# Performance work log

Measured on AMD Instinct MI355X. Metric: run time of the kernel, lower is better.

## Reference

```python
import jax, jax.numpy as jnp
import numpy as np

D = 16  # attention temperature
COEF = 1.0 / float(np.sqrt(D))


def squash2(x, axis=-1):
    sq = jnp.sum(x * x, axis=axis, keepdims=True)
    norm = jnp.sqrt(sq)
    # (1 - 1/exp(||x||)) * x / sqrt(||x||^2 + 1e-8)
    return (1.0 - jnp.exp(-norm)) * x / jnp.sqrt(sq + 1e-8)


def setup_inputs() -> dict:
    key = jax.random.key(0)
    k1, k2, k3 = jax.random.split(key, 3)
    batch, in_caps, in_dim, num_caps, dim_caps = 128, 1024, 16, 16, 16
    x = jax.random.normal(k1, (batch, in_caps, in_dim), dtype=jnp.float32)
    W = 0.01 * jax.random.normal(k2, (1, num_caps, in_caps, dim_caps, in_dim), dtype=jnp.float32)
    B = 0.01 * jax.random.normal(k3, (num_caps, 1, in_caps), dtype=jnp.float32)
    return {"x": x, "W": W, "B": B}


def reference(x, W, B):
    # u_hat[b,n,c,d] = W[n,c,d,:] . x[b,c,:]
    u_hat = jnp.einsum('ncdi,bci->bncd', W[0], x)
    # a = coef * u_hat @ u_hat^T is only consumed via a.sum(dim=-2);
    # sum_r <u_hat[r], u_hat[k]> == <sum_r u_hat[r], u_hat[k]> (same math, no [c,c] matrix)
    scores = COEF * jnp.einsum('bnd,bnkd->bnk', u_hat.sum(axis=2), u_hat)  # [b,n,c]
    c = jax.nn.softmax(scores[:, :, None, :], axis=1)  # softmax over num_caps, [b,n,1,c]
    # s = (c + B) @ u_hat, squeeze row dim
    s = jnp.einsum('bnrc,bncd->bnrd', c + B[None], u_hat)[:, :, 0, :]  # [b,n,d]
    return squash2(s)
```

## Files before the change

kernel.cpp:

```cpp
#include <hip/hip_runtime.h>
#include <math.h>

#define NB 128
#define NC 1024
#define NN 16
#define ND 16
#define NI 16
#define COEF 0.25f

typedef __attribute__((ext_vector_type(8))) short short8;
typedef __attribute__((ext_vector_type(4))) float f32x4;
typedef unsigned short ushort_t;

__device__ __forceinline__ unsigned short f2bf(float f) {
  unsigned int u = __builtin_bit_cast(unsigned int, f);
  u += 0x7fffu + ((u >> 16) & 1u);
  return (unsigned short)(u >> 16);
}

__global__ __launch_bounds__(256) void k_prep(const float4* __restrict__ x,
                                              const float4* __restrict__ W,
                                              ushort_t* __restrict__ xb,
                                              ushort_t* __restrict__ Wb) {
  int id = blockIdx.x * 256 + threadIdx.x;
  const float4* src;
  ushort_t* dst;
  int k;
  if (id < 262144) { src = x; dst = xb; k = id; }
  else { src = W; dst = Wb; k = id - 262144; }
  float4 a = src[2 * k], b = src[2 * k + 1];
  short8 o;
  o[0] = (short)f2bf(a.x); o[1] = (short)f2bf(a.y);
  o[2] = (short)f2bf(a.z); o[3] = (short)f2bf(a.w);
  o[4] = (short)f2bf(b.x); o[5] = (short)f2bf(b.y);
  o[6] = (short)f2bf(b.z); o[7] = (short)f2bf(b.w);
  *(short8*)(dst + (size_t)k * 8) = o;
}

__global__ __launch_bounds__(1024) void k_usum(const ushort_t* __restrict__ xb,
                                               const ushort_t* __restrict__ Wb,
                                               float* __restrict__ usum2) {
  __shared__ f32x4 red[16][64];
  int bx = blockIdx.x;
  int bt = bx >> 5, g = bx & 31;
  int n = g >> 1, h = g & 1;
  int w = threadIdx.x >> 6, l = threadIdx.x & 63;
  int q = l >> 4, b16 = l & 15;
  int c0 = h * 512 + w * 32;
  f32x4 acc[4];
#pragma unroll
  for (int kk = 0; kk < 4; ++kk) acc[kk] = (f32x4){0.f, 0.f, 0.f, 0.f};
#pragma unroll
  for (int kk = 0; kk < 4; ++kk) {
    const ushort_t* ap =
        Wb + (((size_t)(n * NC + c0 + kk * 8 + (q >> 1)) * ND + b16) * NI) + (q & 1) * 8;
    const ushort_t* bp =
        xb + (size_t)(bt * 16 + b16) * (NC * NI) + (c0 + kk * 8 + (q >> 1)) * NI + (q & 1) * 8;
#pragma unroll
    for (int s = 0; s < 4; ++s) {
      short8 av = *(const short8*)ap;
      short8 bv = *(const short8*)bp;
      acc[kk] = __builtin_amdgcn_mfma_f32_16x16x32_bf16(av, bv, acc[kk], 0, 0, 0);
      ap += 2 * ND * NI;
      bp += 2 * NI;
    }
  }
  red[w][l] = (acc[0] + acc[1]) + (acc[2] + acc[3]);
  __syncthreads();
  if (threadIdx.x < 64) {
    f32x4 t = red[0][l];
#pragma unroll
    for (int k = 1; k < 16; ++k) t += red[k][l];
    *(f32x4*)(usum2 + (((size_t)h * NN + n) * NB + bt * 16 + b16) * ND + q * 4) = t;
  }
}

__global__ __launch_bounds__(512, 4) void k_bc(const ushort_t* __restrict__ xb,
                                               const ushort_t* __restrict__ Wb,
                                               const float* __restrict__ usum2,
                                               const float* __restrict__ Bbias,
                                               float* __restrict__ part) {
  __shared__ ushort_t Wl[NN][8][ND][NI];
  __shared__ ushort_t xl[16][136];
  __shared__ float scl[NN][8][16];
  int bx = blockIdx.x;
  int bt = bx >> 7, cc = bx & 127;
  int t = threadIdx.x;
  int w = t >> 6, l = t & 63;
  int q = l >> 4, b16 = l & 15;
  int c0 = cc * 8;
  int n0 = w, n1 = w + 8;

  const float* u0p = usum2 + ((size_t)n0 * NB + bt * 16 + b16) * ND + q * 4;
  f32x4 us0 = *(const f32x4*)u0p + *(const f32x4*)(u0p + (size_t)NN * NB * ND);
  const float* u1p = usum2 + ((size_t)n1 * NB + bt * 16 + b16) * ND + q * 4;
  f32x4 us1 = *(const f32x4*)u1p + *(const f32x4*)(u1p + (size_t)NN * NB * ND);

  {
    ushort_t* Wflat = &Wl[0][0][0][0];
    const ushort_t* Wsrc = Wb + (size_t)c0 * (ND * NI);
#pragma unroll
    for (int r = 0; r < 8; ++r) {
      int g = r * 512 + t;
      int n = g >> 8, rem = g & 255;
      *(short8*)(Wflat + n * 2048 + rem * 8) =
          *(const short8*)(Wsrc + (size_t)n * (NC * ND * NI) + rem * 8);
    }
    if (t < 256) {
      int b = t >> 4, j = t & 15;
      int c = j >> 1, i8 = j & 1;
      *(short8*)(&xl[b][c * 16 + i8 * 8]) =
          *(const short8*)(xb + ((size_t)(bt * 16 + b) * NC + c0 + c) * NI + i8 * 8);
    }
  }
  __syncthreads();

  f32x4 t0[8], t1[8];

#pragma unroll
  for (int c = 0; c < 8; ++c) {
    short8 av = {0, 0, 0, 0, 0, 0, 0, 0};
    short8 bv = {0, 0, 0, 0, 0, 0, 0, 0};
    if (q < 2) {
      av = *(const short8*)(&Wl[n0][c][b16][q * 8]);
      bv = *(const short8*)(&xl[b16][c * 16 + q * 8]);
    }
    f32x4 z = {0.f, 0.f, 0.f, 0.f};
    f32x4 d = __builtin_amdgcn_mfma_f32_16x16x32_bf16(av, bv, z, 0, 0, 0);
    t0[c] = d;
    float v = us0[0] * d[0] + us0[1] * d[1] + us0[2] * d[2] + us0[3] * d[3];
    v += __shfl_xor(v, 16);
    v += __shfl_xor(v, 32);
    if (l < 16) scl[n0][c][l] = COEF * v;
  }
#pragma unroll
  for (int c = 0; c < 8; ++c) {
    short8 av = {0, 0, 0, 0, 0, 0, 0, 0};
    short8 bv = {0, 0, 0, 0, 0, 0, 0, 0};
    if (q < 2) {
      av = *(const short8*)(&Wl[n1][c][b16][q * 8]);
      bv = *(const short8*)(&xl[b16][c * 16 + q * 8]);
    }
    f32x4 z = {0.f, 0.f, 0.f, 0.f};
    f32x4 d = __builtin_amdgcn_mfma_f32_16x16x32_bf16(av, bv, z, 0, 0, 0);
    t1[c] = d;
    float v = us1[0] * d[0] + us1[1] * d[1] + us1[2] * d[2] + us1[3] * d[3];
    v += __shfl_xor(v, 16);
    v += __shfl_xor(v, 32);
    if (l < 16) scl[n1][c][l] = COEF * v;
  }
  __syncthreads();

  if (t < 128) {
    int c = t >> 4, b = t & 15;
    float v[NN];
    float m = -1e30f;
#pragma unroll
    for (int k = 0; k < NN; ++k) {
      v[k] = scl[k][c][b];
      m = fmaxf(m, v[k]);
    }
    float sum = 0.f;
#pragma unroll
    for (int k = 0; k < NN; ++k) {
      v[k] = expf(v[k] - m);
      sum += v[k];
    }
    float inv = 1.0f / sum;
#pragma unroll
    for (int k = 0; k < NN; ++k) {
      scl[k][c][b] = v[k] * inv + Bbias[k * NC + c0 + c];
    }
  }
  __syncthreads();

  f32x4 acc0 = {0.f, 0.f, 0.f, 0.f};
  f32x4 acc1 = {0.f, 0.f, 0.f, 0.f};
#pragma unroll
  for (int c = 0; c < 8; ++c) {
    float cf0 = scl[n0][c][b16];
    float cf1 = scl[n1][c][b16];
    acc0[0] = fmaf(cf0, t0[c][0], acc0[0]);
    acc0[1] = fmaf(cf0, t0[c][1], acc0[1]);
    acc0[2] = fmaf(cf0, t0[c][2], acc0[2]);
    acc0[3] = fmaf(cf0, t0[c][3], acc0[3]);
    acc1[0] = fmaf(cf1, t1[c][0], acc1[0]);
    acc1[1] = fmaf(cf1, t1[c][1], acc1[1]);
    acc1[2] = fmaf(cf1, t1[c][2], acc1[2]);
    acc1[3] = fmaf(cf1, t1[c][3], acc1[3]);
  }
  *(f32x4*)(part + ((size_t)((n0 * 8 + bt) * 128 + cc)) * 256 + b16 * 16 + q * 4) = acc0;
  *(f32x4*)(part + ((size_t)((n1 * 8 + bt) * 128 + cc)) * 256 + b16 * 16 + q * 4) = acc1;
}

__global__ __launch_bounds__(256) void k_fin(const float* __restrict__ part,
                                             float* __restrict__ out) {
  int id2 = blockIdx.x * 256 + threadIdx.x;
  int h = id2 & 1;
  int id = id2 >> 1;
  int dq = id & 3, n = (id >> 2) & 15, b = id >> 6;
  int bt = b >> 4, b16 = b & 15;
  f32x4 sv = {0.f, 0.f, 0.f, 0.f};
  const float* pp = part + ((size_t)((n * 8 + bt) * 128 + h * 64)) * 256 + b16 * 16 + dq * 4;
  for (int k = 0; k < 64; ++k) {
    sv += *(const f32x4*)pp;
    pp += 256;
  }
  sv[0] += __shfl_xor(sv[0], 1);
  sv[1] += __shfl_xor(sv[1], 1);
  sv[2] += __shfl_xor(sv[2], 1);
  sv[3] += __shfl_xor(sv[3], 1);
  float sq = sv[0] * sv[0] + sv[1] * sv[1] + sv[2] * sv[2] + sv[3] * sv[3];
  sq += __shfl_xor(sq, 2);
  sq += __shfl_xor(sq, 4);
  float norm = sqrtf(sq);
  float scale = (1.0f - expf(-norm)) / sqrtf(sq + 1e-8f);
  if (h == 0) {
    f32x4 o = {sv[0] * scale, sv[1] * scale, sv[2] * scale, sv[3] * scale};
    *(f32x4*)(out + (size_t)id * 4) = o;
  }
}

extern "C" void kernel_launch(void* const* d_in, const int* in_sizes, int n_in,
                              void* d_out, int out_size, void* d_ws, size_t ws_size,
                              hipStream_t stream) {
  const float* x = (const float*)d_in[0];
  const float* W = (const float*)d_in[1];
  const float* Bb = (const float*)d_in[2];
  float* out = (float*)d_out;
  float* ws = (float*)d_ws;

  ushort_t* xb = (ushort_t*)ws;
  ushort_t* Wb = (ushort_t*)(ws + 1048576);
  float* part = ws + 1048576 + 2097152;
  float* usum2 = part + 4194304;

  hipLaunchKernelGGL(k_prep, dim3(3072), dim3(256), 0, stream,
                     (const float4*)x, (const float4*)W, xb, Wb);
  hipLaunchKernelGGL(k_usum, dim3(256), dim3(1024), 0, stream, xb, Wb, usum2);
  hipLaunchKernelGGL(k_bc, dim3(1024), dim3(512), 0, stream, xb, Wb, usum2, Bb, part);
  hipLaunchKernelGGL(k_fin, dim3(64), dim3(256), 0, stream, part, out);
}
```

Baseline: 48.42 us.

## Fuse bf16 conversion into usum kernel and restructure final reduction

Drops the separate fp32-to-bf16 prep kernel. The usum kernel now reads fp32 x and W directly, converts them in registers, and writes the bf16 copies for the next stage: W only from the bt==0 blocks and x only from the n==0 blocks. This removes one launch and one full pass over the inputs, but the usum kernel now reads fp32 data redundantly across blocks. The final kernel is also rebuilt to use 128 blocks of 512 threads, with coalesced scalar reads of the partials and a shared-memory combine of the two halves.

```diff
diff --git a/kernel.cpp b/kernel.cpp
--- a/kernel.cpp
+++ b/kernel.cpp
@@ -18,27 +18,19 @@
   return (unsigned short)(u >> 16);
 }
 
-__global__ __launch_bounds__(256) void k_prep(const float4* __restrict__ x,
-                                              const float4* __restrict__ W,
-                                              ushort_t* __restrict__ xb,
-                                              ushort_t* __restrict__ Wb) {
-  int id = blockIdx.x * 256 + threadIdx.x;
-  const float4* src;
-  ushort_t* dst;
-  int k;
-  if (id < 262144) { src = x; dst = xb; k = id; }
-  else { src = W; dst = Wb; k = id - 262144; }
-  float4 a = src[2 * k], b = src[2 * k + 1];
+__device__ __forceinline__ short8 cvt8(float4 a, float4 b) {
   short8 o;
   o[0] = (short)f2bf(a.x); o[1] = (short)f2bf(a.y);
   o[2] = (short)f2bf(a.z); o[3] = (short)f2bf(a.w);
   o[4] = (short)f2bf(b.x); o[5] = (short)f2bf(b.y);
   o[6] = (short)f2bf(b.z); o[7] = (short)f2bf(b.w);
-  *(short8*)(dst + (size_t)k * 8) = o;
-}
-
-__global__ __launch_bounds__(1024) void k_usum(const ushort_t* __restrict__ xb,
-                                               const ushort_t* __restrict__ Wb,
+  return o;
+}
+
+__global__ __launch_bounds__(1024) void k_usum(const float* __restrict__ xf,
+                                               const float* __restrict__ Wf,
+                                               ushort_t* __restrict__ xb,
+                                               ushort_t* __restrict__ Wb,
                                                float* __restrict__ usum2) {
   __shared__ f32x4 red[16][64];
   int bx = blockIdx.x;
@@ -47,22 +39,28 @@
   int w = threadIdx.x >> 6, l = threadIdx.x & 63;
   int q = l >> 4, b16 = l & 15;
   int c0 = h * 512 + w * 32;
+  const bool writeW = (bt == 0);
+  const bool writeX = (n == 0);
   f32x4 acc[4];
 #pragma unroll
   for (int kk = 0; kk < 4; ++kk) acc[kk] = (f32x4){0.f, 0.f, 0.f, 0.f};
 #pragma unroll
   for (int kk = 0; kk < 4; ++kk) {
-    const ushort_t* ap =
-        Wb + (((size_t)(n * NC + c0 + kk * 8 + (q >> 1)) * ND + b16) * NI) + (q & 1) * 8;
-    const ushort_t* bp =
-        xb + (size_t)(bt * 16 + b16) * (NC * NI) + (c0 + kk * 8 + (q >> 1)) * NI + (q & 1) * 8;
+    size_t wo = (((size_t)(n * NC + c0 + kk * 8 + (q >> 1)) * ND + b16) * NI) + (q & 1) * 8;
+    size_t xo = ((size_t)(bt * 16 + b16) * NC + (c0 + kk * 8 + (q >> 1))) * NI + (q & 1) * 8;
 #pragma unroll
     for (int s = 0; s < 4; ++s) {
-      short8 av = *(const short8*)ap;
-      short8 bv = *(const short8*)bp;
+      float4 w0 = *(const float4*)(Wf + wo);
+      float4 w1 = *(const float4*)(Wf + wo + 4);
+      float4 x0 = *(const float4*)(xf + xo);
+      float4 x1 = *(const float4*)(xf + xo + 4);
+      short8 av = cvt8(w0, w1);
+      short8 bv = cvt8(x0, x1);
+      if (writeW) *(short8*)(Wb + wo) = av;
+      if (writeX) *(short8*)(xb + xo) = bv;
       acc[kk] = __builtin_amdgcn_mfma_f32_16x16x32_bf16(av, bv, acc[kk], 0, 0, 0);
-      ap += 2 * ND * NI;
-      bp += 2 * NI;
+      wo += 2 * ND * NI;
+      xo += 2 * NI;
     }
   }
   red[w][l] = (acc[0] + acc[1]) + (acc[2] + acc[3]);
@@ -193,31 +191,33 @@
   *(f32x4*)(part + ((size_t)((n1 * 8 + bt) * 128 + cc)) * 256 + b16 * 16 + q * 4) = acc1;
 }
 
-__global__ __launch_bounds__(256) void k_fin(const float* __restrict__ part,
+__global__ __launch_bounds__(512) void k_fin(const float* __restrict__ part,
                                              float* __restrict__ out) {
-  int id2 = blockIdx.x * 256 + threadIdx.x;
-  int h = id2 & 1;
-  int id = id2 >> 1;
-  int dq = id & 3, n = (id >> 2) & 15, b = id >> 6;
-  int bt = b >> 4, b16 = b & 15;
-  f32x4 sv = {0.f, 0.f, 0.f, 0.f};
-  const float* pp = part + ((size_t)((n * 8 + bt) * 128 + h * 64)) * 256 + b16 * 16 + dq * 4;
-  for (int k = 0; k < 64; ++k) {
-    sv += *(const f32x4*)pp;
+  __shared__ float red[256];
+  int blk = blockIdx.x;
+  int n = blk >> 3, bt = blk & 7;
+  int tid = threadIdx.x;
+  int hh = tid >> 8, t = tid & 255;
+  const float* pp = part + ((size_t)blk * 128 + hh * 64) * 256 + t;
+  float s = 0.f;
+#pragma unroll 8
+  for (int cc = 0; cc < 64; ++cc) {
+    s += *pp;
     pp += 256;
   }
-  sv[0] += __shfl_xor(sv[0], 1);
-  sv[1] += __shfl_xor(sv[1], 1);
-  sv[2] += __shfl_xor(sv[2], 1);
-  sv[3] += __shfl_xor(sv[3], 1);
-  float sq = sv[0] * sv[0] + sv[1] * sv[1] + sv[2] * sv[2] + sv[3] * sv[3];
-  sq += __shfl_xor(sq, 2);
-  sq += __shfl_xor(sq, 4);
-  float norm = sqrtf(sq);
-  float scale = (1.0f - expf(-norm)) / sqrtf(sq + 1e-8f);
-  if (h == 0) {
-    f32x4 o = {sv[0] * scale, sv[1] * scale, sv[2] * scale, sv[3] * scale};
-    *(f32x4*)(out + (size_t)id * 4) = o;
+  if (hh) red[t] = s;
+  __syncthreads();
+  if (tid < 256) {
+    float sv = s + red[t];
+    float sq = sv * sv;
+    sq += __shfl_xor(sq, 1);
+    sq += __shfl_xor(sq, 2);
+    sq += __shfl_xor(sq, 4);
+    sq += __shfl_xor(sq, 8);
+    float norm = sqrtf(sq);
+    float scale = (1.0f - expf(-norm)) / sqrtf(sq + 1e-8f);
+    int b = bt * 16 + (t >> 4), d = t & 15;
+    out[((size_t)b * NN + n) * ND + d] = sv * scale;
   }
 }
 
@@ -235,9 +235,7 @@
   float* part = ws + 1048576 + 2097152;
   float* usum2 = part + 4194304;
 
-  hipLaunchKernelGGL(k_prep, dim3(3072), dim3(256), 0, stream,
-                     (const float4*)x, (const float4*)W, xb, Wb);
-  hipLaunchKernelGGL(k_usum, dim3(256), dim3(1024), 0, stream, xb, Wb, usum2);
+  hipLaunchKernelGGL(k_usum, dim3(256), dim3(1024), 0, stream, x, W, xb, Wb, usum2);
   hipLaunchKernelGGL(k_bc, dim3(1024), dim3(512), 0, stream, xb, Wb, usum2, Bb, part);
-  hipLaunchKernelGGL(k_fin, dim3(64), dim3(256), 0, stream, part, out);
-}
+  hipLaunchKernelGGL(k_fin, dim3(128), dim3(512), 0, stream, part, out);
+}
```

Result: slower. 55.28 us (+14.2%).

## Fuse all stages into one cooperative kernel with grid-wide syncs

Applied to the files above, without the earlier changes.

Replaces the four-kernel pipeline (bf16 prep, u_hat sum, scores/softmax/weighted sum, final reduction and squash) with a single cooperative kernel of 256 blocks. Each block converts its W and x tile to bf16 in LDS once and reuses it for the u_hat-sum pass, the score pass and the weighted-sum pass, with grid.sync between the cross-block reductions. This removes the launch overheads and the global round trips of the bf16 copies. In exchange it adds three grid barriers and recomputes the MFMA products instead of keeping them in registers. The four-kernel path is kept as a fallback if the cooperative launch fails.

```diff
diff --git a/kernel.cpp b/kernel.cpp
--- a/kernel.cpp
+++ b/kernel.cpp
@@ -1,5 +1,8 @@
 #include <hip/hip_runtime.h>
+#include <hip/hip_cooperative_groups.h>
 #include <math.h>
+
+namespace cg = cooperative_groups;
 
 #define NB 128
 #define NC 1024
@@ -16,6 +19,197 @@
   unsigned int u = __builtin_bit_cast(unsigned int, f);
   u += 0x7fffu + ((u >> 16) & 1u);
   return (unsigned short)(u >> 16);
+}
+__device__ __forceinline__ short8 cvt8(float4 a, float4 b) {
+  short8 o;
+  o[0] = (short)f2bf(a.x); o[1] = (short)f2bf(a.y);
+  o[2] = (short)f2bf(a.z); o[3] = (short)f2bf(a.w);
+  o[4] = (short)f2bf(b.x); o[5] = (short)f2bf(b.y);
+  o[6] = (short)f2bf(b.z); o[7] = (short)f2bf(b.w);
+  return o;
+}
+
+__global__ __launch_bounds__(1024) void k_all(const float* __restrict__ xf,
+                                              const float* __restrict__ Wf,
+                                              const float* __restrict__ Bbias,
+                                              float* __restrict__ out,
+                                              float* __restrict__ upart,
+                                              float* __restrict__ usum) {
+  __shared__ ushort_t Wl[NN][8][ND][NI];
+  __shared__ ushort_t xl[64][136];
+  __shared__ float scl[NN][8][64];
+  __shared__ float red2[8][132];
+
+  cg::grid_group grid = cg::this_grid();
+  const int blk = blockIdx.x;
+  const int btg = blk >> 7, cc = blk & 127;
+  const int t = threadIdx.x;
+  const int w = t >> 6, l = t & 63;
+  const int q = l >> 4, b16 = l & 15;
+  const int c0 = cc * 8;
+  const int n = w;
+
+  {
+    ushort_t* Wflat = &Wl[0][0][0][0];
+#pragma unroll
+    for (int r = 0; r < 4; ++r) {
+      int f = r * 1024 + t;
+      int nn = f >> 8, rem = f & 255;
+      const float* src = Wf + ((size_t)(nn * NC + c0)) * 256 + rem * 8;
+      float4 a = *(const float4*)src;
+      float4 b = *(const float4*)(src + 4);
+      *(short8*)(Wflat + nn * 2048 + rem * 8) = cvt8(a, b);
+    }
+    int row = t >> 4, rem = t & 15;
+    const float* src = xf + ((size_t)(btg * 64 + row) * NC + c0) * 16 + rem * 8;
+    float4 a = *(const float4*)src;
+    float4 b = *(const float4*)(src + 4);
+    *(short8*)(&xl[row][rem * 8]) = cvt8(a, b);
+  }
+  __syncthreads();
+
+#pragma unroll
+  for (int g2 = 0; g2 < 4; ++g2) {
+    f32x4 acc = {0.f, 0.f, 0.f, 0.f};
+#pragma unroll
+    for (int kk = 0; kk < 4; ++kk) {
+      short8 av = *(const short8*)(&Wl[n][kk * 2 + (q >> 1)][b16][(q & 1) * 8]);
+      short8 bv = *(const short8*)(&xl[g2 * 16 + b16][(kk * 2 + (q >> 1)) * 16 + (q & 1) * 8]);
+      acc = __builtin_amdgcn_mfma_f32_16x16x32_bf16(av, bv, acc, 0, 0, 0);
+    }
+    int row = n * 8 + btg * 4 + g2;
+    *(f32x4*)(upart + ((size_t)row * 128 + cc) * 256 + b16 * 16 + q * 4) = acc;
+  }
+  grid.sync();
+
+  {
+    int row = blk >> 1;
+    int ph = (blk & 1) * 128;
+    int j = t >> 7, ol = t & 127;
+    const float* pp = upart + ((size_t)row * 128 + j * 16) * 256 + ph + ol;
+    float s = 0.f;
+#pragma unroll
+    for (int s16 = 0; s16 < 16; ++s16) { s += *pp; pp += 256; }
+    red2[j][ol] = s;
+    __syncthreads();
+    if (t < 128) {
+      float tot = 0.f;
+#pragma unroll
+      for (int jj = 0; jj < 8; ++jj) tot += red2[jj][t];
+      int pos = ph + t;
+      int nn = row >> 3, bt16 = row & 7;
+      int b = bt16 * 16 + (pos >> 4), d = pos & 15;
+      usum[((size_t)nn * NB + b) * ND + d] = tot;
+    }
+  }
+  grid.sync();
+
+  {
+    f32x4 us[4];
+#pragma unroll
+    for (int g2 = 0; g2 < 4; ++g2)
+      us[g2] = *(const f32x4*)(usum + ((size_t)n * NB + btg * 64 + g2 * 16 + b16) * ND + q * 4);
+#pragma unroll
+    for (int c = 0; c < 8; ++c) {
+#pragma unroll
+      for (int g2 = 0; g2 < 4; ++g2) {
+        short8 av = {0, 0, 0, 0, 0, 0, 0, 0};
+        short8 bv = {0, 0, 0, 0, 0, 0, 0, 0};
+        if (q < 2) {
+          av = *(const short8*)(&Wl[n][c][b16][q * 8]);
+          bv = *(const short8*)(&xl[g2 * 16 + b16][c * 16 + q * 8]);
+        }
+        f32x4 z = {0.f, 0.f, 0.f, 0.f};
+        f32x4 d = __builtin_amdgcn_mfma_f32_16x16x32_bf16(av, bv, z, 0, 0, 0);
+        float v = us[g2][0] * d[0] + us[g2][1] * d[1] + us[g2][2] * d[2] + us[g2][3] * d[3];
+        v += __shfl_xor(v, 16);
+        v += __shfl_xor(v, 32);
+        if (l < 16) scl[n][c][g2 * 16 + l] = COEF * v;
+      }
+    }
+  }
+  __syncthreads();
+
+  if (t < 512) {
+    int c = t >> 6, b = t & 63;
+    float v[NN];
+    float m = -1e30f;
+#pragma unroll
+    for (int k = 0; k < NN; ++k) {
+      v[k] = scl[k][c][b];
+      m = fmaxf(m, v[k]);
+    }
+    float sum = 0.f;
+#pragma unroll
+    for (int k = 0; k < NN; ++k) {
+      v[k] = expf(v[k] - m);
+      sum += v[k];
+    }
+    float inv = 1.0f / sum;
+#pragma unroll
+    for (int k = 0; k < NN; ++k) scl[k][c][b] = v[k] * inv + Bbias[k * NC + c0 + c];
+  }
+  __syncthreads();
+
+  {
+    f32x4 acc[4];
+#pragma unroll
+    for (int g2 = 0; g2 < 4; ++g2) acc[g2] = (f32x4){0.f, 0.f, 0.f, 0.f};
+#pragma unroll
+    for (int c = 0; c < 8; ++c) {
+#pragma unroll
+      for (int g2 = 0; g2 < 4; ++g2) {
+        short8 av = {0, 0, 0, 0, 0, 0, 0, 0};
+        short8 bv = {0, 0, 0, 0, 0, 0, 0, 0};
+        if (q < 2) {
+          av = *(const short8*)(&Wl[n][c][b16][q * 8]);
+          bv = *(const short8*)(&xl[g2 * 16 + b16][c * 16 + q * 8]);
+        }
+        f32x4 z = {0.f, 0.f, 0.f, 0.f};
+        f32x4 d = __builtin_amdgcn_mfma_f32_16x16x32_bf16(av, bv, z, 0, 0, 0);
+        float cf = scl[n][c][g2 * 16 + b16];
+        acc[g2][0] = fmaf(cf, d[0], acc[g2][0]);
+        acc[g2][1] = fmaf(cf, d[1], acc[g2][1]);
+        acc[g2][2] = fmaf(cf, d[2], acc[g2][2]);
+        acc[g2][3] = fmaf(cf, d[3], acc[g2][3]);
+      }
+    }
+#pragma unroll
+    for (int g2 = 0; g2 < 4; ++g2) {
+      int row = n * 8 + btg * 4 + g2;
+      *(f32x4*)(upart + ((size_t)row * 128 + cc) * 256 + b16 * 16 + q * 4) = acc[g2];
+    }
+  }
+  grid.sync();
+
+  {
+    int row = blk >> 1;
+    int ph = (blk & 1) * 128;
+    int j = t >> 7, ol = t & 127;
+    const float* pp = upart + ((size_t)row * 128 + j * 16) * 256 + ph + ol;
+    float s = 0.f;
+#pragma unroll
+    for (int s16 = 0; s16 < 16; ++s16) { s += *pp; pp += 256; }
+    __syncthreads();
+    red2[j][ol] = s;
+    __syncthreads();
+    if (t < 128) {
+      float sv = 0.f;
+#pragma unroll
+      for (int jj = 0; jj < 8; ++jj) sv += red2[jj][t];
+      float sq = sv * sv;
+      sq += __shfl_xor(sq, 1);
+      sq += __shfl_xor(sq, 2);
+      sq += __shfl_xor(sq, 4);
+      sq += __shfl_xor(sq, 8);
+      float norm = sqrtf(sq);
+      float scale = (1.0f - expf(-norm)) / sqrtf(sq + 1e-8f);
+      int pos = ph + t;
+      int nn = row >> 3, bt16 = row & 7;
+      int b = bt16 * 16 + (pos >> 4), d = pos & 15;
+      out[((size_t)b * NN + nn) * ND + d] = sv * scale;
+    }
+  }
 }
 
 __global__ __launch_bounds__(256) void k_prep(const float4* __restrict__ x,
@@ -29,12 +223,7 @@
   if (id < 262144) { src = x; dst = xb; k = id; }
   else { src = W; dst = Wb; k = id - 262144; }
   float4 a = src[2 * k], b = src[2 * k + 1];
-  short8 o;
-  o[0] = (short)f2bf(a.x); o[1] = (short)f2bf(a.y);
-  o[2] = (short)f2bf(a.z); o[3] = (short)f2bf(a.w);
-  o[4] = (short)f2bf(b.x); o[5] = (short)f2bf(b.y);
-  o[6] = (short)f2bf(b.z); o[7] = (short)f2bf(b.w);
-  *(short8*)(dst + (size_t)k * 8) = o;
+  *(short8*)(dst + (size_t)k * 8) = cvt8(a, b);
 }
 
 __global__ __launch_bounds__(1024) void k_usum(const ushort_t* __restrict__ xb,
@@ -68,10 +257,10 @@
   red[w][l] = (acc[0] + acc[1]) + (acc[2] + acc[3]);
   __syncthreads();
   if (threadIdx.x < 64) {
-    f32x4 t = red[0][l];
-#pragma unroll
-    for (int k = 1; k < 16; ++k) t += red[k][l];
-    *(f32x4*)(usum2 + (((size_t)h * NN + n) * NB + bt * 16 + b16) * ND + q * 4) = t;
+    f32x4 tt = red[0][l];
+#pragma unroll
+    for (int k = 1; k < 16; ++k) tt += red[k][l];
+    *(f32x4*)(usum2 + (((size_t)h * NN + n) * NB + bt * 16 + b16) * ND + q * 4) = tt;
   }
 }
 
@@ -90,21 +279,19 @@
   int q = l >> 4, b16 = l & 15;
   int c0 = cc * 8;
   int n0 = w, n1 = w + 8;
-
   const float* u0p = usum2 + ((size_t)n0 * NB + bt * 16 + b16) * ND + q * 4;
   f32x4 us0 = *(const f32x4*)u0p + *(const f32x4*)(u0p + (size_t)NN * NB * ND);
   const float* u1p = usum2 + ((size_t)n1 * NB + bt * 16 + b16) * ND + q * 4;
   f32x4 us1 = *(const f32x4*)u1p + *(const f32x4*)(u1p + (size_t)NN * NB * ND);
-
   {
     ushort_t* Wflat = &Wl[0][0][0][0];
     const ushort_t* Wsrc = Wb + (size_t)c0 * (ND * NI);
 #pragma unroll
     for (int r = 0; r < 8; ++r) {
       int g = r * 512 + t;
-      int n = g >> 8, rem = g & 255;
-      *(short8*)(Wflat + n * 2048 + rem * 8) =
-          *(const short8*)(Wsrc + (size_t)n * (NC * ND * NI) + rem * 8);
+      int nn = g >> 8, rem = g & 255;
+      *(short8*)(Wflat + nn * 2048 + rem * 8) =
+          *(const short8*)(Wsrc + (size_t)nn * (NC * ND * NI) + rem * 8);
     }
     if (t < 256) {
       int b = t >> 4, j = t & 15;
@@ -114,9 +301,7 @@
     }
   }
   __syncthreads();
-
   f32x4 t0[8], t1[8];
-
 #pragma unroll
   for (int c = 0; c < 8; ++c) {
     short8 av = {0, 0, 0, 0, 0, 0, 0, 0};
@@ -150,7 +335,6 @@
     if (l < 16) scl[n1][c][l] = COEF * v;
   }
   __syncthreads();
-
   if (t < 128) {
     int c = t >> 4, b = t & 15;
     float v[NN];
@@ -168,12 +352,9 @@
     }
     float inv = 1.0f / sum;
 #pragma unroll
-    for (int k = 0; k < NN; ++k) {
-      scl[k][c][b] = v[k] * inv + Bbias[k * NC + c0 + c];
-    }
-  }
-  __syncthreads();
-
+    for (int k = 0; k < NN; ++k) scl[k][c][b] = v[k] * inv + Bbias[k * NC + c0 + c];
+  }
+  __syncthreads();
   f32x4 acc0 = {0.f, 0.f, 0.f, 0.f};
   f32x4 acc1 = {0.f, 0.f, 0.f, 0.f};
 #pragma unroll
@@ -230,14 +411,23 @@
   float* out = (float*)d_out;
   float* ws = (float*)d_ws;
 
-  ushort_t* xb = (ushort_t*)ws;
-  ushort_t* Wb = (ushort_t*)(ws + 1048576);
-  float* part = ws + 1048576 + 2097152;
+  float* upart = ws;
+  float* usum = ws + 4194304;
+  float* fb = ws + 4227072;
+  ushort_t* xb = (ushort_t*)fb;
+  ushort_t* Wb = (ushort_t*)(fb + 1048576);
+  float* part = fb + 1048576 + 2097152;
   float* usum2 = part + 4194304;
 
-  hipLaunchKernelGGL(k_prep, dim3(3072), dim3(256), 0, stream,
-                     (const float4*)x, (const float4*)W, xb, Wb);
-  hipLaunchKernelGGL(k_usum, dim3(256), dim3(1024), 0, stream, xb, Wb, usum2);
-  hipLaunchKernelGGL(k_bc, dim3(1024), dim3(512), 0, stream, xb, Wb, usum2, Bb, part);
-  hipLaunchKernelGGL(k_fin, dim3(64), dim3(256), 0, stream, part, out);
-}
+  void* args[] = {(void*)&x, (void*)&W, (void*)&Bb, (void*)&out,
+                  (void*)&upart, (void*)&usum};
+  hipError_t e = hipLaunchCooperativeKernel((const void*)k_all, dim3(256), dim3(1024),
+                                            args, 0, stream);
+  if (e != hipSuccess) {
+    hipLaunchKernelGGL(k_prep, dim3(3072), dim3(256), 0, stream,
+                       (const float4*)x, (const float4*)W, xb, Wb);
+    hipLaunchKernelGGL(k_usum, dim3(256), dim3(1024), 0, stream, xb, Wb, usum2);
+    hipLaunchKernelGGL(k_bc, dim3(1024), dim3(512), 0, stream, xb, Wb, usum2, Bb, part);
+    hipLaunchKernelGGL(k_fin, dim3(64), dim3(256), 0, stream, part, out);
+  }
+}
```

Measured after the change: 167.0 us. 245% more time.

## Store partial sums in bf16 and split final reduction across four lanes

Applied to the files above, without the earlier changes.

The per-tile partial results written by k_bc are converted to bf16 before being stored. This halves the bytes written and then read back through the 16 MB partial buffer. k_fin now splits each 128-tile reduction over four lanes instead of two and launches twice as many blocks, with an unrolled inner loop. Rounding each partial to bf16 adds error to the accumulated capsule vectors.

```diff
diff --git a/kernel.cpp b/kernel.cpp
--- a/kernel.cpp
+++ b/kernel.cpp
@@ -9,6 +9,7 @@
 #define COEF 0.25f
 
 typedef __attribute__((ext_vector_type(8))) short short8;
+typedef __attribute__((ext_vector_type(4))) short short4v;
 typedef __attribute__((ext_vector_type(4))) float f32x4;
 typedef unsigned short ushort_t;
 
@@ -16,6 +17,10 @@
   unsigned int u = __builtin_bit_cast(unsigned int, f);
   u += 0x7fffu + ((u >> 16) & 1u);
   return (unsigned short)(u >> 16);
+}
+__device__ __forceinline__ float bf2f(unsigned short u) {
+  unsigned int v = ((unsigned int)u) << 16;
+  return __builtin_bit_cast(float, v);
 }
 
 __global__ __launch_bounds__(256) void k_prep(const float4* __restrict__ x,
@@ -79,7 +84,7 @@
                                                const ushort_t* __restrict__ Wb,
                                                const float* __restrict__ usum2,
                                                const float* __restrict__ Bbias,
-                                               float* __restrict__ part) {
+                                               ushort_t* __restrict__ part) {
   __shared__ ushort_t Wl[NN][8][ND][NI];
   __shared__ ushort_t xl[16][136];
   __shared__ float scl[NN][8][16];
@@ -189,30 +194,41 @@
     acc1[2] = fmaf(cf1, t1[c][2], acc1[2]);
     acc1[3] = fmaf(cf1, t1[c][3], acc1[3]);
   }
-  *(f32x4*)(part + ((size_t)((n0 * 8 + bt) * 128 + cc)) * 256 + b16 * 16 + q * 4) = acc0;
-  *(f32x4*)(part + ((size_t)((n1 * 8 + bt) * 128 + cc)) * 256 + b16 * 16 + q * 4) = acc1;
-}
-
-__global__ __launch_bounds__(256) void k_fin(const float* __restrict__ part,
+  short4v p0 = {(short)f2bf(acc0[0]), (short)f2bf(acc0[1]),
+                (short)f2bf(acc0[2]), (short)f2bf(acc0[3])};
+  short4v p1 = {(short)f2bf(acc1[0]), (short)f2bf(acc1[1]),
+                (short)f2bf(acc1[2]), (short)f2bf(acc1[3])};
+  *(short4v*)(part + ((size_t)((n0 * 8 + bt) * 128 + cc)) * 256 + b16 * 16 + q * 4) = p0;
+  *(short4v*)(part + ((size_t)((n1 * 8 + bt) * 128 + cc)) * 256 + b16 * 16 + q * 4) = p1;
+}
+
+__global__ __launch_bounds__(256) void k_fin(const ushort_t* __restrict__ part,
                                              float* __restrict__ out) {
   int id2 = blockIdx.x * 256 + threadIdx.x;
-  int h = id2 & 1;
-  int id = id2 >> 1;
+  int h = id2 & 3;
+  int id = id2 >> 2;
   int dq = id & 3, n = (id >> 2) & 15, b = id >> 6;
   int bt = b >> 4, b16 = b & 15;
   f32x4 sv = {0.f, 0.f, 0.f, 0.f};
-  const float* pp = part + ((size_t)((n * 8 + bt) * 128 + h * 64)) * 256 + b16 * 16 + dq * 4;
-  for (int k = 0; k < 64; ++k) {
-    sv += *(const f32x4*)pp;
+  const ushort_t* pp =
+      part + ((size_t)((n * 8 + bt) * 128 + h * 32)) * 256 + b16 * 16 + dq * 4;
+#pragma unroll 8
+  for (int k = 0; k < 32; ++k) {
+    short4v p = *(const short4v*)pp;
+    sv[0] += bf2f((unsigned short)p[0]);
+    sv[1] += bf2f((unsigned short)p[1]);
+    sv[2] += bf2f((unsigned short)p[2]);
+    sv[3] += bf2f((unsigned short)p[3]);
     pp += 256;
   }
-  sv[0] += __shfl_xor(sv[0], 1);
-  sv[1] += __shfl_xor(sv[1], 1);
-  sv[2] += __shfl_xor(sv[2], 1);
-  sv[3] += __shfl_xor(sv[3], 1);
+#pragma unroll
+  for (int j = 0; j < 4; ++j) {
+    sv[j] += __shfl_xor(sv[j], 1);
+    sv[j] += __shfl_xor(sv[j], 2);
+  }
   float sq = sv[0] * sv[0] + sv[1] * sv[1] + sv[2] * sv[2] + sv[3] * sv[3];
-  sq += __shfl_xor(sq, 2);
   sq += __shfl_xor(sq, 4);
+  sq += __shfl_xor(sq, 8);
   float norm = sqrtf(sq);
   float scale = (1.0f - expf(-norm)) / sqrtf(sq + 1e-8f);
   if (h == 0) {
@@ -232,12 +248,12 @@
 
   ushort_t* xb = (ushort_t*)ws;
   ushort_t* Wb = (ushort_t*)(ws + 1048576);
-  float* part = ws + 1048576 + 2097152;
-  float* usum2 = part + 4194304;
+  ushort_t* part = (ushort_t*)(ws + 1048576 + 2097152);
+  float* usum2 = ws + 1048576 + 2097152 + 2097152;
 
   hipLaunchKernelGGL(k_prep, dim3(3072), dim3(256), 0, stream,
                      (const float4*)x, (const float4*)W, xb, Wb);
   hipLaunchKernelGGL(k_usum, dim3(256), dim3(1024), 0, stream, xb, Wb, usum2);
   hipLaunchKernelGGL(k_bc, dim3(1024), dim3(512), 0, stream, xb, Wb, usum2, Bb, part);
-  hipLaunchKernelGGL(k_fin, dim3(64), dim3(256), 0, stream, part, out);
-}
+  hipLaunchKernelGGL(k_fin, dim3(128), dim3(256), 0, stream, part, out);
+}
```

Measured after the change: 45.87 us. 1.06x faster.
